# Kernel tuning notes

Measured on AMD Instinct MI355X. Metric: run time of the kernel, lower is better.

Reference implementation:

```python
import jax, jax.numpy as jnp
import numpy as np

XBITS = 8  # bitconfig['xbits']


def quantize(x, bits=XBITS):
    """Per-tensor dynamic fixed-point fake-quant.
    topk(|x|, k=len, largest=False).max() == max(|x|), so the 'percentile' is a no-op.
    scale = 2**(bits - ceil(log2(max|x|)) - 1); clamp(round(x*scale), -t, t)/scale.
    """
    thresh = float(2 ** (bits - 1) - 1)
    max_abs = jnp.max(jnp.abs(x))
    # get_scale returns 0 on log2 domain error (threshold <= 0)
    exp = jnp.where(max_abs > 0, jnp.ceil(jnp.log2(max_abs)), jnp.zeros((), x.dtype))
    scale = jnp.exp2(jnp.asarray(bits, x.dtype) - exp - 1)
    return jnp.clip(jnp.round(x * scale), -thresh, thresh) / scale


def setup_inputs() -> dict:
    key = jax.random.key(0)
    k1, k2, k3 = jax.random.split(key, 3)
    N, D_in, D_out = 65536, 1024, 1024
    x = jax.random.normal(k1, (N, D_in), dtype=jnp.float32)
    weight = jax.random.normal(k2, (D_out, D_in), dtype=jnp.float32) * (1.0 / np.sqrt(D_in))
    bias = jax.random.normal(k3, (D_out,), dtype=jnp.float32) * (1.0 / np.sqrt(D_in))
    return {"x": x, "weight": weight, "bias": bias}


def reference(x, weight, bias):
    # FixedLinearFunction.forward: quantize both operands, matmul; bias is NOT added.
    q_x = quantize(x)
    q_w = quantize(weight)
    return q_x @ q_w.T  # [N, D_out]
```

## Files before the change

### kernel.cpp

```cpp
#include <hip/hip_runtime.h>
#include <stdint.h>

typedef int v4i  __attribute__((ext_vector_type(4)));
typedef int v16i __attribute__((ext_vector_type(16)));

__device__ __forceinline__ void async_load16(const void* g, void* l) {
    auto gp = (const __attribute__((address_space(1))) unsigned int*)(uintptr_t)g;
    auto lp = (__attribute__((address_space(3))) unsigned int*)(unsigned int)(uintptr_t)l;
    __builtin_amdgcn_global_load_lds(gp, lp, 16, 0, 0);
}

__global__ void k_init(unsigned* bits) {
    if (threadIdx.x < 2) bits[threadIdx.x] = 0u;
}

__global__ void k_absmax(const float4* __restrict__ x, int n4x, int nbx,
                         const float4* __restrict__ w, int n4w, int nbw,
                         unsigned* __restrict__ bits) {
    const float4* in;
    int n4, b, nb;
    unsigned* ob;
    if ((int)blockIdx.x < nbx) { in = x; n4 = n4x; b = blockIdx.x; nb = nbx; ob = bits; }
    else { in = w; n4 = n4w; b = blockIdx.x - nbx; nb = nbw; ob = bits + 1; }
    float m0 = 0.f, m1 = 0.f;
    int stride = nb * blockDim.x * 2;
    for (int i = b * blockDim.x * 2 + threadIdx.x; i < n4; i += stride) {
        float4 v = in[i];
        m0 = fmaxf(m0, fmaxf(fmaxf(fabsf(v.x), fabsf(v.y)),
                             fmaxf(fabsf(v.z), fabsf(v.w))));
        int j = i + blockDim.x;
        if (j < n4) {
            float4 u = in[j];
            m1 = fmaxf(m1, fmaxf(fmaxf(fabsf(u.x), fabsf(u.y)),
                                 fmaxf(fabsf(u.z), fabsf(u.w))));
        }
    }
    float m = fmaxf(m0, m1);
    #pragma unroll
    for (int off = 32; off > 0; off >>= 1)
        m = fmaxf(m, __shfl_down(m, off, 64));
    __shared__ float red[4];
    int lane = threadIdx.x & 63, wv = threadIdx.x >> 6;
    if (lane == 0) red[wv] = m;
    __syncthreads();
    if (threadIdx.x == 0) {
        m = fmaxf(fmaxf(red[0], red[1]), fmaxf(red[2], red[3]));
        atomicMax(ob, __float_as_uint(m));
    }
}

__global__ void k_scales(const unsigned* __restrict__ bits, float* __restrict__ sc) {
    float s[2];
    for (int i = 0; i < 2; ++i) {
        float m = __uint_as_float(bits[i]);
        int ex = 0;
        if (m > 0.0f) {
            int e;
            float f = frexpf(m, &e);
            ex = (f == 0.5f) ? (e - 1) : e;
        }
        s[i] = ldexpf(1.0f, 7 - ex);
    }
    sc[0] = s[0]; sc[1] = s[1];
    sc[2] = 1.0f / (s[0] * s[1]);
}

__global__ void k_quant(const float4* __restrict__ x, int* __restrict__ qx, int n4x, int nbx,
                        const float4* __restrict__ w, int* __restrict__ qw, int n4w, int nbw,
                        const float* __restrict__ scp) {
    const float4* in; int* out;
    int n4, b, nb; float s;
    if ((int)blockIdx.x < nbx) { in = x; out = qx; n4 = n4x; b = blockIdx.x; nb = nbx; s = scp[0]; }
    else { in = w; out = qw; n4 = n4w; b = blockIdx.x - nbx; nb = nbw; s = scp[1]; }
    int stride = nb * blockDim.x;
    for (int i = b * blockDim.x + threadIdx.x; i < n4; i += stride) {
        float4 v = in[i];
        int qa = (int)rintf(v.x * s); qa = qa > 127 ? 127 : (qa < -127 ? -127 : qa);
        int qb = (int)rintf(v.y * s); qb = qb > 127 ? 127 : (qb < -127 ? -127 : qb);
        int qc = (int)rintf(v.z * s); qc = qc > 127 ? 127 : (qc < -127 ? -127 : qc);
        int qd = (int)rintf(v.w * s); qd = qd > 127 ? 127 : (qd < -127 ? -127 : qd);
        out[i] = (qa & 0xff) | ((qb & 0xff) << 8) | ((qc & 0xff) << 16) | (qd << 24);
    }
}

__global__ __launch_bounds__(256, 3) void k_gemm(const signed char* __restrict__ A,
                                                 const signed char* __restrict__ B,
                                                 float* __restrict__ out,
                                                 const float* __restrict__ scp) {
    __shared__ __align__(16) signed char sm[2][2][8192];
    const int tid  = threadIdx.x;
    const int lane = tid & 63;
    const int wave = tid >> 6;
    const int wm   = wave & 1;
    const int wn   = wave >> 1;
    const int m0   = blockIdx.y * 128;
    const int n0   = blockIdx.x * 128;
    const int l31  = lane & 31;
    const int lhi  = lane >> 5;

    v16i acc[2][2];
    #pragma unroll
    for (int a = 0; a < 2; ++a)
        #pragma unroll
        for (int b = 0; b < 2; ++b)
            #pragma unroll
            for (int i = 0; i < 16; ++i) acc[a][b][i] = 0;

    const int L0 = tid, L1 = tid + 256;
    const signed char* gA0 = A + (size_t)(m0 + (L0 & 127)) * 1024 + (L0 >> 7) * 16;
    const signed char* gA1 = A + (size_t)(m0 + (L1 & 127)) * 1024 + (L1 >> 7) * 16;
    const signed char* gB0 = B + (size_t)(n0 + (L0 & 127)) * 1024 + (L0 >> 7) * 16;
    const signed char* gB1 = B + (size_t)(n0 + (L1 & 127)) * 1024 + (L1 >> 7) * 16;

    async_load16(gA0, &sm[0][0][L0 * 16]);
    async_load16(gA1, &sm[0][0][L1 * 16]);
    async_load16(gB0, &sm[0][1][L0 * 16]);
    async_load16(gB1, &sm[0][1][L1 * 16]);

    for (int it = 0; it < 16; ++it) {
        __syncthreads();
        if (it < 15) {
            const int k0 = (it + 1) * 64;
            const int nb = (it + 1) & 1;
            async_load16(gA0 + k0, &sm[nb][0][L0 * 16]);
            async_load16(gA1 + k0, &sm[nb][0][L1 * 16]);
            async_load16(gB0 + k0, &sm[nb][1][L0 * 16]);
            async_load16(gB1 + k0, &sm[nb][1][L1 * 16]);
        }
        const signed char* As = sm[it & 1][0];
        const signed char* Bs = sm[it & 1][1];
        #pragma unroll
        for (int kc = 0; kc < 2; ++kc) {
            const int c = kc * 2 + lhi;
            v4i a0 = *(const v4i*)(As + (c * 128 + wm * 64 +      l31) * 16);
            v4i a1 = *(const v4i*)(As + (c * 128 + wm * 64 + 32 + l31) * 16);
            v4i b0 = *(const v4i*)(Bs + (c * 128 + wn * 64 +      l31) * 16);
            v4i b1 = *(const v4i*)(Bs + (c * 128 + wn * 64 + 32 + l31) * 16);
            acc[0][0] = __builtin_amdgcn_mfma_i32_32x32x32_i8(a0, b0, acc[0][0], 0, 0, 0);
            acc[0][1] = __builtin_amdgcn_mfma_i32_32x32x32_i8(a0, b1, acc[0][1], 0, 0, 0);
            acc[1][0] = __builtin_amdgcn_mfma_i32_32x32x32_i8(a1, b0, acc[1][0], 0, 0, 0);
            acc[1][1] = __builtin_amdgcn_mfma_i32_32x32x32_i8(a1, b1, acc[1][1], 0, 0, 0);
        }
    }

    const float inv = scp[2];
    #pragma unroll
    for (int tm = 0; tm < 2; ++tm)
        #pragma unroll
        for (int tn = 0; tn < 2; ++tn)
            #pragma unroll
            for (int r = 0; r < 16; ++r) {
                int row = m0 + wm * 64 + tm * 32 + (r & 3) + 8 * (r >> 2) + 4 * lhi;
                int col = n0 + wn * 64 + tn * 32 + l31;
                out[(size_t)row * 1024 + col] = (float)acc[tm][tn][r] * inv;
            }
}

extern "C" void kernel_launch(void* const* d_in, const int* in_sizes, int n_in,
                              void* d_out, int out_size, void* d_ws, size_t ws_size,
                              hipStream_t stream) {
    const float* x = (const float*)d_in[0];
    const float* w = (const float*)d_in[1];
    float* out = (float*)d_out;

    const int NX = 65536 * 1024;
    const int NW = 1024 * 1024;

    char* ws = (char*)d_ws;
    unsigned* bits = (unsigned*)ws;
    float* sc = (float*)(ws + 8);
    signed char* qx = (signed char*)(ws + 256);
    signed char* qw = qx + (size_t)NX;

    const int NBX_A = 8192, NBW_A = 128;
    const int NBX_Q = 8192, NBW_Q = 128;

    k_init<<<1, 64, 0, stream>>>(bits);
    k_absmax<<<NBX_A + NBW_A, 256, 0, stream>>>(
        (const float4*)x, NX / 4, NBX_A, (const float4*)w, NW / 4, NBW_A, bits);
    k_scales<<<1, 1, 0, stream>>>(bits, sc);
    k_quant<<<NBX_Q + NBW_Q, 256, 0, stream>>>(
        (const float4*)x, (int*)qx, NX / 4, NBX_Q,
        (const float4*)w, (int*)qw, NW / 4, NBW_Q, sc);

    dim3 grid(1024 / 128, 65536 / 128);
    k_gemm<<<grid, 256, 0, stream>>>(qx, qw, out, sc);
}
```

Before: 658.7 us.

## Triple-buffer GEMM LDS loads, remap block order, replace atomic absmax with partials

The GEMM moves from a double-buffered to a triple-buffered LDS pipeline. It prefetches two K-steps ahead and uses explicit vmcnt waits with split barriers, so global loads overlap more compute. Blocks are remapped from a 1D grid so that groups of consecutive blocks cover all N tiles for nearby M tiles, which may improve L2 reuse. The absmax reduction now writes per-block partials that a 256-thread scales kernel reduces, removing the init kernel and the atomics. The cost is more LDS per block (48KB), which may limit occupancy under launch_bounds(256,3).

```diff
diff --git a/kernel.cpp b/kernel.cpp
--- a/kernel.cpp
+++ b/kernel.cpp
@@ -10,18 +10,13 @@
     __builtin_amdgcn_global_load_lds(gp, lp, 16, 0, 0);
 }
 
-__global__ void k_init(unsigned* bits) {
-    if (threadIdx.x < 2) bits[threadIdx.x] = 0u;
-}
-
 __global__ void k_absmax(const float4* __restrict__ x, int n4x, int nbx,
-                         const float4* __restrict__ w, int n4w, int nbw,
-                         unsigned* __restrict__ bits) {
+                         const float4* __restrict__ w, int n4w,
+                         float* __restrict__ part) {
     const float4* in;
     int n4, b, nb;
-    unsigned* ob;
-    if ((int)blockIdx.x < nbx) { in = x; n4 = n4x; b = blockIdx.x; nb = nbx; ob = bits; }
-    else { in = w; n4 = n4w; b = blockIdx.x - nbx; nb = nbw; ob = bits + 1; }
+    if ((int)blockIdx.x < nbx) { in = x; n4 = n4x; b = blockIdx.x; nb = nbx; }
+    else { in = w; n4 = n4w; b = blockIdx.x - nbx; nb = gridDim.x - nbx; }
     float m0 = 0.f, m1 = 0.f;
     int stride = nb * blockDim.x * 2;
     for (int i = b * blockDim.x * 2 + threadIdx.x; i < n4; i += stride) {
@@ -43,35 +38,49 @@
     int lane = threadIdx.x & 63, wv = threadIdx.x >> 6;
     if (lane == 0) red[wv] = m;
     __syncthreads();
+    if (threadIdx.x == 0)
+        part[blockIdx.x] = fmaxf(fmaxf(red[0], red[1]), fmaxf(red[2], red[3]));
+}
+
+__global__ void k_scales(const float* __restrict__ part, int nbx, int nbw,
+                         float* __restrict__ sc) {
+    float mx = 0.f, mw = 0.f;
+    for (int i = threadIdx.x; i < nbx; i += 256) mx = fmaxf(mx, part[i]);
+    for (int i = threadIdx.x; i < nbw; i += 256) mw = fmaxf(mw, part[nbx + i]);
+    #pragma unroll
+    for (int off = 32; off > 0; off >>= 1) {
+        mx = fmaxf(mx, __shfl_down(mx, off, 64));
+        mw = fmaxf(mw, __shfl_down(mw, off, 64));
+    }
+    __shared__ float rx[4], rw[4];
+    int lane = threadIdx.x & 63, wv = threadIdx.x >> 6;
+    if (lane == 0) { rx[wv] = mx; rw[wv] = mw; }
+    __syncthreads();
     if (threadIdx.x == 0) {
-        m = fmaxf(fmaxf(red[0], red[1]), fmaxf(red[2], red[3]));
-        atomicMax(ob, __float_as_uint(m));
-    }
-}
-
-__global__ void k_scales(const unsigned* __restrict__ bits, float* __restrict__ sc) {
-    float s[2];
-    for (int i = 0; i < 2; ++i) {
-        float m = __uint_as_float(bits[i]);
-        int ex = 0;
-        if (m > 0.0f) {
-            int e;
-            float f = frexpf(m, &e);
-            ex = (f == 0.5f) ? (e - 1) : e;
-        }
-        s[i] = ldexpf(1.0f, 7 - ex);
-    }
-    sc[0] = s[0]; sc[1] = s[1];
-    sc[2] = 1.0f / (s[0] * s[1]);
+        float m[2] = { fmaxf(fmaxf(rx[0], rx[1]), fmaxf(rx[2], rx[3])),
+                       fmaxf(fmaxf(rw[0], rw[1]), fmaxf(rw[2], rw[3])) };
+        float s[2];
+        for (int i = 0; i < 2; ++i) {
+            int ex = 0;
+            if (m[i] > 0.0f) {
+                int e;
+                float f = frexpf(m[i], &e);
+                ex = (f == 0.5f) ? (e - 1) : e;
+            }
+            s[i] = ldexpf(1.0f, 7 - ex);
+        }
+        sc[0] = s[0]; sc[1] = s[1];
+        sc[2] = 1.0f / (s[0] * s[1]);
+    }
 }
 
 __global__ void k_quant(const float4* __restrict__ x, int* __restrict__ qx, int n4x, int nbx,
-                        const float4* __restrict__ w, int* __restrict__ qw, int n4w, int nbw,
+                        const float4* __restrict__ w, int* __restrict__ qw, int n4w,
                         const float* __restrict__ scp) {
     const float4* in; int* out;
     int n4, b, nb; float s;
     if ((int)blockIdx.x < nbx) { in = x; out = qx; n4 = n4x; b = blockIdx.x; nb = nbx; s = scp[0]; }
-    else { in = w; out = qw; n4 = n4w; b = blockIdx.x - nbx; nb = nbw; s = scp[1]; }
+    else { in = w; out = qw; n4 = n4w; b = blockIdx.x - nbx; nb = gridDim.x - nbx; s = scp[1]; }
     int stride = nb * blockDim.x;
     for (int i = b * blockDim.x + threadIdx.x; i < n4; i += stride) {
         float4 v = in[i];
@@ -87,14 +96,17 @@
                                                  const signed char* __restrict__ B,
                                                  float* __restrict__ out,
                                                  const float* __restrict__ scp) {
-    __shared__ __align__(16) signed char sm[2][2][8192];
+    __shared__ __align__(16) signed char sm[3][2][8192];
     const int tid  = threadIdx.x;
     const int lane = tid & 63;
     const int wave = tid >> 6;
     const int wm   = wave & 1;
     const int wn   = wave >> 1;
-    const int m0   = blockIdx.y * 128;
-    const int n0   = blockIdx.x * 128;
+    const int bl   = blockIdx.x;
+    const int g    = bl & 7;
+    const int j    = bl >> 3;
+    const int n0   = (j & 7) * 128;
+    const int m0   = (g * 64 + (j >> 3)) * 128;
     const int l31  = lane & 31;
     const int lhi  = lane >> 5;
 
@@ -111,24 +123,35 @@
     const signed char* gA1 = A + (size_t)(m0 + (L1 & 127)) * 1024 + (L1 >> 7) * 16;
     const signed char* gB0 = B + (size_t)(n0 + (L0 & 127)) * 1024 + (L0 >> 7) * 16;
     const signed char* gB1 = B + (size_t)(n0 + (L1 & 127)) * 1024 + (L1 >> 7) * 16;
-
-    async_load16(gA0, &sm[0][0][L0 * 16]);
-    async_load16(gA1, &sm[0][0][L1 * 16]);
-    async_load16(gB0, &sm[0][1][L0 * 16]);
-    async_load16(gB1, &sm[0][1][L1 * 16]);
+    const int o0 = L0 * 16, o1 = L1 * 16;
+
+    async_load16(gA0,      &sm[0][0][o0]);
+    async_load16(gA1,      &sm[0][0][o1]);
+    async_load16(gB0,      &sm[0][1][o0]);
+    async_load16(gB1,      &sm[0][1][o1]);
+    async_load16(gA0 + 64, &sm[1][0][o0]);
+    async_load16(gA1 + 64, &sm[1][0][o1]);
+    async_load16(gB0 + 64, &sm[1][1][o0]);
+    async_load16(gB1 + 64, &sm[1][1][o1]);
 
     for (int it = 0; it < 16; ++it) {
-        __syncthreads();
-        if (it < 15) {
-            const int k0 = (it + 1) * 64;
-            const int nb = (it + 1) & 1;
-            async_load16(gA0 + k0, &sm[nb][0][L0 * 16]);
-            async_load16(gA1 + k0, &sm[nb][0][L1 * 16]);
-            async_load16(gB0 + k0, &sm[nb][1][L0 * 16]);
-            async_load16(gB1 + k0, &sm[nb][1][L1 * 16]);
-        }
-        const signed char* As = sm[it & 1][0];
-        const signed char* Bs = sm[it & 1][1];
+        __builtin_amdgcn_s_barrier();
+        if (it < 14) {
+            const int k0 = (it + 2) * 64;
+            const int s  = (it + 2) % 3;
+            async_load16(gA0 + k0, &sm[s][0][o0]);
+            async_load16(gA1 + k0, &sm[s][0][o1]);
+            async_load16(gB0 + k0, &sm[s][1][o0]);
+            async_load16(gB1 + k0, &sm[s][1][o1]);
+            asm volatile("s_waitcnt vmcnt(8)" ::: "memory");
+        } else if (it == 14) {
+            asm volatile("s_waitcnt vmcnt(4)" ::: "memory");
+        } else {
+            asm volatile("s_waitcnt vmcnt(0)" ::: "memory");
+        }
+        __builtin_amdgcn_s_barrier();
+        const signed char* As = &sm[it % 3][0][0];
+        const signed char* Bs = &sm[it % 3][1][0];
         #pragma unroll
         for (int kc = 0; kc < 2; ++kc) {
             const int c = kc * 2 + lhi;
@@ -167,22 +190,18 @@
     const int NW = 1024 * 1024;
 
     char* ws = (char*)d_ws;
-    unsigned* bits = (unsigned*)ws;
-    float* sc = (float*)(ws + 8);
-    signed char* qx = (signed char*)(ws + 256);
+    float* sc   = (float*)ws;
+    float* part = (float*)(ws + 256);
+    signed char* qx = (signed char*)(ws + 65536);
     signed char* qw = qx + (size_t)NX;
 
-    const int NBX_A = 8192, NBW_A = 128;
-    const int NBX_Q = 8192, NBW_Q = 128;
-
-    k_init<<<1, 64, 0, stream>>>(bits);
-    k_absmax<<<NBX_A + NBW_A, 256, 0, stream>>>(
-        (const float4*)x, NX / 4, NBX_A, (const float4*)w, NW / 4, NBW_A, bits);
-    k_scales<<<1, 1, 0, stream>>>(bits, sc);
-    k_quant<<<NBX_Q + NBW_Q, 256, 0, stream>>>(
-        (const float4*)x, (int*)qx, NX / 4, NBX_Q,
-        (const float4*)w, (int*)qw, NW / 4, NBW_Q, sc);
-
-    dim3 grid(1024 / 128, 65536 / 128);
-    k_gemm<<<grid, 256, 0, stream>>>(qx, qw, out, sc);
-}
+    const int NBX = 8192, NBW = 128;
+
+    k_absmax<<<NBX + NBW, 256, 0, stream>>>(
+        (const float4*)x, NX / 4, NBX, (const float4*)w, NW / 4, part);
+    k_scales<<<1, 256, 0, stream>>>(part, NBX, NBW, sc);
+    k_quant<<<NBX + NBW, 256, 0, stream>>>(
+        (const float4*)x, (int*)qx, NX / 4, NBX,
+        (const float4*)w, (int*)qw, NW / 4, sc);
+    k_gemm<<<4096, 256, 0, stream>>>(qx, qw, out, sc);
+}
```

New measurement: 639.1 us. -3.0%, faster.
